# Kernel optimization log

Measured on AMD Instinct MI355X. Metric: run time of the kernel, lower is better.

## Reference

```python
import jax, jax.numpy as jnp
import numpy as np

NUM_EXPERTS = 8
TOP_K = 2
CAPACITY_FACTOR = 1.25


def setup_inputs() -> dict:
    key = jax.random.key(0)
    ks = jax.random.split(key, 5)
    B, S, D, H, E = 4, 2048, 1024, 2048, NUM_EXPERTS
    scale = 0.02
    return {
        "x": jax.random.normal(ks[0], (B, S, D), dtype=jnp.float32),
        "gate_w": jax.random.normal(ks[1], (E, D), dtype=jnp.float32) * scale,
        "gate_proj_w": jax.random.normal(ks[2], (E, H, D), dtype=jnp.float32) * scale,
        "up_proj_w": jax.random.normal(ks[3], (E, H, D), dtype=jnp.float32) * scale,
        "down_proj_w": jax.random.normal(ks[4], (E, D, H), dtype=jnp.float32) * scale,
    }


def reference(x, gate_w, gate_proj_w, up_proj_w, down_proj_w):
    B, S, D = x.shape
    E, K = NUM_EXPERTS, TOP_K
    T = B * S
    xf = x.reshape(T, D)

    # Router: softmax over expert logits, then top-k (eval mode: no aux loss)
    logits = xf @ gate_w.T                      # (T, E)
    probs = jax.nn.softmax(logits, axis=-1)
    top_p, top_i = jax.lax.top_k(probs, K)      # (T, K)
    w = top_p / (jnp.sum(top_p, axis=-1, keepdims=True) + 1e-9)  # (T, K)

    # Capacity drop: per (k, expert), keep only the first `capacity` tokens
    # in token order (matches torch loop which truncates nonzero indices).
    capacity = int(CAPACITY_FACTOR * T / E)
    oh = jax.nn.one_hot(top_i, E, dtype=jnp.int32)        # (T, K, E)
    rank = jnp.cumsum(oh, axis=0) - 1                     # rank within (k, e)
    my_rank = jnp.sum(rank * oh, axis=-1)                 # (T, K)
    keep = (my_rank < capacity).astype(w.dtype)

    # Combined per-token per-expert weight (dropped tokens get 0)
    comb = jnp.einsum("tk,tke->te", w * keep, oh.astype(w.dtype))  # (T, E)

    # Per-expert dense SwiGLU; zero-weight tokens contribute nothing,
    # which matches the masked gather/scatter-add of the original.
    out = jnp.zeros_like(xf)
    for e in range(E):
        g = jax.nn.silu(xf @ gate_proj_w[e].T)   # (T, H)
        u = xf @ up_proj_w[e].T                  # (T, H)
        y = (g * u) @ down_proj_w[e].T           # (T, D)
        out = out + comb[:, e:e + 1] * y
    return out.reshape(B, S, D)
```

## Files before the change

### kernel.cpp

```cpp
#include <hip/hip_runtime.h>
#include <hip/hip_bf16.h>
#include <stdint.h>

#define T_TOK 8192
#define D_DIM 1024
#define H_DIM 2048
#define E_NUM 8
#define CAP   1280
#define CAP2  2560

#define BM 128
#define BN 128
#define BK 32

typedef __attribute__((ext_vector_type(8))) short short8;
typedef __attribute__((ext_vector_type(4))) float float4v;
typedef __attribute__((address_space(1))) const unsigned int gu32;
typedef __attribute__((address_space(3))) unsigned int lu32;

static __device__ __forceinline__ unsigned short f2bf(float f) {
    unsigned int u = __float_as_uint(f);
    unsigned int r = (u + 0x7FFFu + ((u >> 16) & 1u)) >> 16;
    return (unsigned short)r;
}

static __device__ __forceinline__ void store4bf(unsigned short* d, float4 v) {
    union { unsigned short u[4]; uint2 q; } pk;
    pk.u[0] = f2bf(v.x); pk.u[1] = f2bf(v.y);
    pk.u[2] = f2bf(v.z); pk.u[3] = f2bf(v.w);
    *(uint2*)d = pk.q;
}

__global__ __launch_bounds__(256) void convert_all_k(
    const float* __restrict__ wg, const float* __restrict__ wu,
    const float* __restrict__ wd, const float* __restrict__ x,
    unsigned short* __restrict__ wgbf, unsigned short* __restrict__ wubf,
    unsigned short* __restrict__ wdbf, unsigned short* __restrict__ xbf) {
    const int W4 = E_NUM * H_DIM * D_DIM / 4;
    const int X4 = T_TOK * D_DIM / 4;
    const int total = 3 * W4 + X4;
    const int stride = gridDim.x * 256;
    for (int i = blockIdx.x * 256 + threadIdx.x; i < total; i += stride) {
        const float* s; unsigned short* d; int j;
        if (i < W4)            { s = wg; d = wgbf; j = i; }
        else if (i < 2 * W4)   { s = wu; d = wubf; j = i - W4; }
        else if (i < 3 * W4)   { s = wd; d = wdbf; j = i - 2 * W4; }
        else                   { s = x;  d = xbf;  j = i - 3 * W4; }
        store4bf(d + (size_t)j * 4, ((const float4*)s)[j]);
    }
}

__global__ __launch_bounds__(256) void router_k(
    const float* __restrict__ x, const float* __restrict__ gw,
    int* __restrict__ topi, float* __restrict__ topw) {
    const int t = blockIdx.x * 4 + (threadIdx.x >> 6);
    const int lane = threadIdx.x & 63;
    const float* xr = x + (size_t)t * D_DIM;

    float p[E_NUM];
#pragma unroll
    for (int e = 0; e < E_NUM; ++e) p[e] = 0.f;
#pragma unroll
    for (int c = 0; c < 4; ++c) {
        const int idx = c * 256 + lane * 4;
        const float4 xv = *(const float4*)(xr + idx);
#pragma unroll
        for (int e = 0; e < E_NUM; ++e) {
            const float4 gv = *(const float4*)(gw + e * D_DIM + idx);
            p[e] += xv.x * gv.x + xv.y * gv.y + xv.z * gv.z + xv.w * gv.w;
        }
    }
#pragma unroll
    for (int e = 0; e < E_NUM; ++e) {
        float v = p[e];
#pragma unroll
        for (int off = 32; off >= 1; off >>= 1) v += __shfl_xor(v, off);
        p[e] = v;
    }
    if (lane == 0) {
        float mx = p[0];
#pragma unroll
        for (int e = 1; e < E_NUM; ++e) mx = fmaxf(mx, p[e]);
        float pe[E_NUM]; float s = 0.f;
#pragma unroll
        for (int e = 0; e < E_NUM; ++e) { pe[e] = expf(p[e] - mx); s += pe[e]; }
        const float inv = 1.f / s;
        int i0 = 0;
#pragma unroll
        for (int e = 1; e < E_NUM; ++e) if (pe[e] > pe[i0]) i0 = e;
        int i1 = -1;
#pragma unroll
        for (int e = 0; e < E_NUM; ++e) {
            if (e == i0) continue;
            if (i1 < 0 || pe[e] > pe[i1]) i1 = e;
        }
        const float p0 = pe[i0] * inv, p1 = pe[i1] * inv;
        const float wn = 1.f / (p0 + p1 + 1e-9f);
        topi[t * 2 + 0] = i0; topi[t * 2 + 1] = i1;
        topw[t * 2 + 0] = p0 * wn; topw[t * 2 + 1] = p1 * wn;
    }
}

__global__ __launch_bounds__(1024) void assign_k(
    const int* __restrict__ topi, const float* __restrict__ topw,
    int* __restrict__ tok_list, float* __restrict__ w_list,
    int* __restrict__ n_tot) {
    __shared__ unsigned char topiL[T_TOK * 2];
    __shared__ int kept[2][E_NUM];
    __shared__ int ntotL[E_NUM];
    const int tid = threadIdx.x;
    const int wid = tid >> 6, lane = tid & 63;
    const int k = wid >> 3, e = wid & 7;
    const uint64_t lt = (1ull << lane) - 1ull;

    for (int i = tid; i < T_TOK * 2 / 4; i += 1024) {
        const int4 v = ((const int4*)topi)[i];
        uchar4 b;
        b.x = (unsigned char)v.x; b.y = (unsigned char)v.y;
        b.z = (unsigned char)v.z; b.w = (unsigned char)v.w;
        ((uchar4*)topiL)[i] = b;
    }
    __syncthreads();

    int total = 0;
    for (int base = 0; base < T_TOK; base += 64) {
        const int idx = topiL[(base + lane) * 2 + k];
        total += __popcll(__ballot(idx == e));
    }
    if (lane == 0) kept[k][e] = min(total, CAP);
    __syncthreads();
    if (tid < E_NUM) {
        ntotL[tid] = kept[0][tid] + kept[1][tid];
        n_tot[tid] = ntotL[tid];
    }
    const int myBase = e * CAP2 + (k ? kept[0][e] : 0);

    int running = 0, keptRun = 0;
    for (int base = 0; base < T_TOK; base += 64) {
        const int t = base + lane;
        const bool pred = (topiL[t * 2 + k] == e);
        const uint64_t m = __ballot(pred);
        const int rank = running + __popcll(m & lt);
        const bool keep = pred && (rank < CAP);
        const uint64_t km = __ballot(keep);
        if (keep) {
            const int slot = myBase + keptRun + __popcll(km & lt);
            tok_list[slot] = t;
            w_list[slot] = topw[t * 2 + k];
        }
        running += __popcll(m);
        keptRun += __popcll(km);
    }
    __syncthreads();
    for (int s = tid; s < E_NUM * CAP2; s += 1024) {
        const int ee = s / CAP2, ls = s - ee * CAP2;
        if (ls >= ntotL[ee]) { tok_list[s] = 0; w_list[s] = 0.f; }
    }
}

__global__ __launch_bounds__(256, 2) void gateup_bf_k(
    const unsigned short* __restrict__ xbf,
    const unsigned short* __restrict__ wgbf, const unsigned short* __restrict__ wubf,
    const int* __restrict__ tok_list, const int* __restrict__ n_tot,
    unsigned short* __restrict__ h_ws, int e0) {
    const int ez = blockIdx.z;
    const int e = e0 + ez;
    const int m0 = blockIdx.y * BM;
    if (m0 >= n_tot[e]) return;
    const int n0 = blockIdx.x * BN;

    __shared__ __align__(1024) unsigned short smem[12288];

    const int tid = threadIdx.x, wid = tid >> 6, lane = tid & 63;

    const unsigned short* gsrc[6];
    int ldsoff[6];
#pragma unroll
    for (int i = 0; i < 6; ++i) {
        const int f = (wid * 6 + i) * 64 + lane;
        const unsigned short* g;
        if (f < 512) {
            const int row = f >> 2;
            const int tok = tok_list[e * CAP2 + m0 + row];
            g = xbf + (size_t)tok * D_DIM + (f & 3) * 8;
        } else if (f < 1024) {
            const int r = (f - 512) >> 2;
            g = wgbf + ((size_t)e * H_DIM + n0 + r) * D_DIM + (f & 3) * 8;
        } else {
            const int r = (f - 1024) >> 2;
            g = wubf + ((size_t)e * H_DIM + n0 + r) * D_DIM + (f & 3) * 8;
        }
        gsrc[i] = g;
        ldsoff[i] = (wid * 6 + i) * 1024;
    }

    float4v accg[4][4], accu[4][4];
#pragma unroll
    for (int i = 0; i < 4; ++i)
#pragma unroll
        for (int j = 0; j < 4; ++j) {
            accg[i][j] = (float4v){0.f, 0.f, 0.f, 0.f};
            accu[i][j] = (float4v){0.f, 0.f, 0.f, 0.f};
        }

    const int wm = (wid & 1) * 64, wn = (wid >> 1) * 64;
    const int frow = lane & 15;
    const int fk = (lane >> 4) * 8;

    for (int k0 = 0; k0 < D_DIM; k0 += BK) {
#pragma unroll
        for (int i = 0; i < 6; ++i)
            __builtin_amdgcn_global_load_lds(
                (gu32*)(gsrc[i] + k0),
                (lu32*)((char*)smem + ldsoff[i]), 16, 0, 0);
        __syncthreads();

        short8 af[4], bgf[4], buf[4];
#pragma unroll
        for (int i = 0; i < 4; ++i)
            af[i] = *(const short8*)&smem[(wm + i * 16 + frow) * 32 + fk];
#pragma unroll
        for (int j = 0; j < 4; ++j) {
            bgf[j] = *(const short8*)&smem[4096 + (wn + j * 16 + frow) * 32 + fk];
            buf[j] = *(const short8*)&smem[8192 + (wn + j * 16 + frow) * 32 + fk];
        }
#pragma unroll
        for (int i = 0; i < 4; ++i)
#pragma unroll
            for (int j = 0; j < 4; ++j) {
                accg[i][j] = __builtin_amdgcn_mfma_f32_16x16x32_bf16(af[i], bgf[j], accg[i][j], 0, 0, 0);
                accu[i][j] = __builtin_amdgcn_mfma_f32_16x16x32_bf16(af[i], buf[j], accu[i][j], 0, 0, 0);
            }
        __syncthreads();
    }

    const int col = lane & 15, rbase = (lane >> 4) * 4;
#pragma unroll
    for (int i = 0; i < 4; ++i)
#pragma unroll
        for (int j = 0; j < 4; ++j)
#pragma unroll
            for (int r = 0; r < 4; ++r) {
                const float g = accg[i][j][r];
                const float u = accu[i][j][r];
                const float hv = (g / (1.f + __expf(-g))) * u;
                const int m = wm + i * 16 + rbase + r;
                const int n = wn + j * 16 + col;
                h_ws[((size_t)ez * CAP2 + m0 + m) * H_DIM + (n0 + n)] = f2bf(hv);
            }
}

__global__ __launch_bounds__(256, 2) void down_bf_k(
    const unsigned short* __restrict__ h_ws, const unsigned short* __restrict__ wdbf,
    const int* __restrict__ tok_list, const float* __restrict__ w_list,
    const int* __restrict__ n_tot, float* __restrict__ out, int e0) {
    const int ez = blockIdx.z;
    const int e = e0 + ez;
    const int m0 = blockIdx.y * BM;
    if (m0 >= n_tot[e]) return;
    const int n0 = blockIdx.x * BN;

    __shared__ __align__(1024) unsigned short smem[16384];
    __shared__ int tokL[BM];
    __shared__ float wL[BM];

    const int tid = threadIdx.x, wid = tid >> 6, lane = tid & 63;
    if (tid < BM) {
        tokL[tid] = tok_list[e * CAP2 + m0 + tid];
        wL[tid] = w_list[e * CAP2 + m0 + tid];
    }

    const unsigned short* gsrc[8];
    int ldsoff[8];
#pragma unroll
    for (int i = 0; i < 8; ++i) {
        const int f = (wid * 8 + i) * 64 + lane;
        const unsigned short* g;
        if (f < 1024) {
            const int r = f >> 3, c = (f & 7) ^ (r & 7);
            g = h_ws + ((size_t)ez * CAP2 + m0 + r) * H_DIM + c * 8;
        } else {
            const int fr = f - 1024;
            const int r = fr >> 3, c = (fr & 7) ^ (r & 7);
            g = wdbf + ((size_t)e * D_DIM + n0 + r) * H_DIM + c * 8;
        }
        gsrc[i] = g;
        ldsoff[i] = (wid * 8 + i) * 1024;
    }

    float4v acc[4][4];
#pragma unroll
    for (int i = 0; i < 4; ++i)
#pragma unroll
        for (int j = 0; j < 4; ++j) acc[i][j] = (float4v){0.f, 0.f, 0.f, 0.f};

    const int wm = (wid & 1) * 64, wn = (wid >> 1) * 64;
    const int frow = lane & 15;
    const int quad = lane >> 4;

    for (int k0 = 0; k0 < H_DIM; k0 += 64) {
#pragma unroll
        for (int i = 0; i < 8; ++i)
            __builtin_amdgcn_global_load_lds(
                (gu32*)(gsrc[i] + k0),
                (lu32*)((char*)smem + ldsoff[i]), 16, 0, 0);
        __syncthreads();

        short8 af[2][4], bf[2][4];
#pragma unroll
        for (int s = 0; s < 2; ++s) {
            const int c = s * 4 + quad;
#pragma unroll
            for (int i = 0; i < 4; ++i) {
                const int row = wm + i * 16 + frow;
                af[s][i] = *(const short8*)&smem[(row * 8 + (c ^ (row & 7))) * 8];
            }
#pragma unroll
            for (int j = 0; j < 4; ++j) {
                const int row = wn + j * 16 + frow;
                bf[s][j] = *(const short8*)&smem[8192 + (row * 8 + (c ^ (row & 7))) * 8];
            }
        }
#pragma unroll
        for (int s = 0; s < 2; ++s)
#pragma unroll
            for (int i = 0; i < 4; ++i)
#pragma unroll
                for (int j = 0; j < 4; ++j)
                    acc[i][j] = __builtin_amdgcn_mfma_f32_16x16x32_bf16(af[s][i], bf[s][j], acc[i][j], 0, 0, 0);
        __syncthreads();
    }

    const int col = lane & 15, rbase = (lane >> 4) * 4;
#pragma unroll
    for (int i = 0; i < 4; ++i)
#pragma unroll
        for (int j = 0; j < 4; ++j)
#pragma unroll
            for (int r = 0; r < 4; ++r) {
                const int m = wm + i * 16 + rbase + r;
                const int n = wn + j * 16 + col;
                const float v = acc[i][j][r] * wL[m];
                unsafeAtomicAdd(&out[(size_t)tokL[m] * D_DIM + n0 + n], v);
            }
}

__global__ __launch_bounds__(256, 2) void gateup_legacy_k(
    const float* __restrict__ x,
    const float* __restrict__ wg_all, const float* __restrict__ wu_all,
    const int* __restrict__ tok_list, const int* __restrict__ n_tot,
    unsigned short* __restrict__ h_ws, int e0) {
    const int ez = blockIdx.z;
    const int e = e0 + ez;
    const int m0 = blockIdx.y * BM;
    if (m0 >= n_tot[e]) return;
    const int n0 = blockIdx.x * BN;

    __shared__ __align__(16) unsigned short As[BM][BK];
    __shared__ __align__(16) unsigned short Bg[BN][BK];
    __shared__ __align__(16) unsigned short Bu[BN][BK];
    __shared__ int tokL[BM];

    const int tid = threadIdx.x;
    if (tid < BM) tokL[tid] = tok_list[e * CAP2 + m0 + tid];
    __syncthreads();

    const float* wg = wg_all + (size_t)e * H_DIM * D_DIM;
    const float* wu = wu_all + (size_t)e * H_DIM * D_DIM;

    const float* aSrc[4]; const float* gSrc[4]; const float* uSrc[4];
    unsigned short* aDst[4]; unsigned short* gDst[4]; unsigned short* uDst[4];
#pragma unroll
    for (int it = 0; it < 4; ++it) {
        const int fid = it * 256 + tid;
        const int row = fid >> 3;
        const int c4 = (fid & 7) * 4;
        aSrc[it] = x + (size_t)tokL[row] * D_DIM + c4;
        gSrc[it] = wg + (size_t)(n0 + row) * D_DIM + c4;
        uSrc[it] = wu + (size_t)(n0 + row) * D_DIM + c4;
        aDst[it] = &As[row][c4];
        gDst[it] = &Bg[row][c4];
        uDst[it] = &Bu[row][c4];
    }

    float4v accg[4][4], accu[4][4];
#pragma unroll
    for (int i = 0; i < 4; ++i)
#pragma unroll
        for (int j = 0; j < 4; ++j) {
            accg[i][j] = (float4v){0.f, 0.f, 0.f, 0.f};
            accu[i][j] = (float4v){0.f, 0.f, 0.f, 0.f};
        }

    const int wid = tid >> 6, lane = tid & 63;
    const int wm = (wid & 1) * 64, wn = (wid >> 1) * 64;
    const int frow = lane & 15;
    const int fk = (lane >> 4) * 8;

    for (int k0 = 0; k0 < D_DIM; k0 += BK) {
#pragma unroll
        for (int it = 0; it < 4; ++it) {
            store4bf(aDst[it], *(const float4*)(aSrc[it] + k0));
            store4bf(gDst[it], *(const float4*)(gSrc[it] + k0));
            store4bf(uDst[it], *(const float4*)(uSrc[it] + k0));
        }
        __syncthreads();
        short8 af[4], bgf[4], buf[4];
#pragma unroll
        for (int i = 0; i < 4; ++i)
            af[i] = *(const short8*)&As[wm + i * 16 + frow][fk];
#pragma unroll
        for (int j = 0; j < 4; ++j) {
            bgf[j] = *(const short8*)&Bg[wn + j * 16 + frow][fk];
            buf[j] = *(const short8*)&Bu[wn + j * 16 + frow][fk];
        }
#pragma unroll
        for (int i = 0; i < 4; ++i)
#pragma unroll
            for (int j = 0; j < 4; ++j) {
                accg[i][j] = __builtin_amdgcn_mfma_f32_16x16x32_bf16(af[i], bgf[j], accg[i][j], 0, 0, 0);
                accu[i][j] = __builtin_amdgcn_mfma_f32_16x16x32_bf16(af[i], buf[j], accu[i][j], 0, 0, 0);
            }
        __syncthreads();
    }

    const int col = lane & 15, rbase = (lane >> 4) * 4;
#pragma unroll
    for (int i = 0; i < 4; ++i)
#pragma unroll
        for (int j = 0; j < 4; ++j)
#pragma unroll
            for (int r = 0; r < 4; ++r) {
                const float g = accg[i][j][r];
                const float u = accu[i][j][r];
                const float hv = (g / (1.f + __expf(-g))) * u;
                const int m = wm + i * 16 + rbase + r;
                const int n = wn + j * 16 + col;
                h_ws[((size_t)ez * CAP2 + m0 + m) * H_DIM + (n0 + n)] = f2bf(hv);
            }
}

__global__ __launch_bounds__(256, 2) void down_legacy_k(
    const unsigned short* __restrict__ h_ws, const float* __restrict__ wd_all,
    const int* __restrict__ tok_list, const float* __restrict__ w_list,
    const int* __restrict__ n_tot, float* __restrict__ out, int e0) {
    const int ez = blockIdx.z;
    const int e = e0 + ez;
    const int m0 = blockIdx.y * BM;
    if (m0 >= n_tot[e]) return;
    const int n0 = blockIdx.x * BN;

    __shared__ __align__(16) unsigned short As[BM][BK];
    __shared__ __align__(16) unsigned short Bs[BN][BK];
    __shared__ int tokL[BM];
    __shared__ float wL[BM];

    const int tid = threadIdx.x;
    if (tid < BM) {
        tokL[tid] = tok_list[e * CAP2 + m0 + tid];
        wL[tid] = w_list[e * CAP2 + m0 + tid];
    }
    __syncthreads();

    const unsigned short* hA = h_ws + ((size_t)ez * CAP2 + m0) * H_DIM;
    const float* wd = wd_all + (size_t)e * D_DIM * H_DIM;

    const unsigned short* aSrc[2]; unsigned short* aDst[2];
#pragma unroll
    for (int it = 0; it < 2; ++it) {
        const int fid = it * 256 + tid;
        const int row = fid >> 2;
        const int c8 = (fid & 3) * 8;
        aSrc[it] = hA + (size_t)row * H_DIM + c8;
        aDst[it] = &As[row][c8];
    }
    const float* bSrc[4]; unsigned short* bDst[4];
#pragma unroll
    for (int it = 0; it < 4; ++it) {
        const int fid = it * 256 + tid;
        const int row = fid >> 3;
        const int c4 = (fid & 7) * 4;
        bSrc[it] = wd + (size_t)(n0 + row) * H_DIM + c4;
        bDst[it] = &Bs[row][c4];
    }

    float4v acc[4][4];
#pragma unroll
    for (int i = 0; i < 4; ++i)
#pragma unroll
        for (int j = 0; j < 4; ++j) acc[i][j] = (float4v){0.f, 0.f, 0.f, 0.f};

    const int wid = tid >> 6, lane = tid & 63;
    const int wm = (wid & 1) * 64, wn = (wid >> 1) * 64;
    const int frow = lane & 15;
    const int fk = (lane >> 4) * 8;

    for (int k0 = 0; k0 < H_DIM; k0 += BK) {
#pragma unroll
        for (int it = 0; it < 2; ++it)
            *(uint4*)aDst[it] = *(const uint4*)(aSrc[it] + k0);
#pragma unroll
        for (int it = 0; it < 4; ++it)
            store4bf(bDst[it], *(const float4*)(bSrc[it] + k0));
        __syncthreads();
        short8 af[4], bf[4];
#pragma unroll
        for (int i = 0; i < 4; ++i)
            af[i] = *(const short8*)&As[wm + i * 16 + frow][fk];
#pragma unroll
        for (int j = 0; j < 4; ++j)
            bf[j] = *(const short8*)&Bs[wn + j * 16 + frow][fk];
#pragma unroll
        for (int i = 0; i < 4; ++i)
#pragma unroll
            for (int j = 0; j < 4; ++j)
                acc[i][j] = __builtin_amdgcn_mfma_f32_16x16x32_bf16(af[i], bf[j], acc[i][j], 0, 0, 0);
        __syncthreads();
    }

    const int col = lane & 15, rbase = (lane >> 4) * 4;
#pragma unroll
    for (int i = 0; i < 4; ++i)
#pragma unroll
        for (int j = 0; j < 4; ++j)
#pragma unroll
            for (int r = 0; r < 4; ++r) {
                const int m = wm + i * 16 + rbase + r;
                const int n = wn + j * 16 + col;
                const float v = acc[i][j][r] * wL[m];
                unsafeAtomicAdd(&out[(size_t)tokL[m] * D_DIM + n0 + n], v);
            }
}

extern "C" void kernel_launch(void* const* d_in, const int* in_sizes, int n_in,
                              void* d_out, int out_size, void* d_ws, size_t ws_size,
                              hipStream_t stream) {
    const float* x        = (const float*)d_in[0];
    const float* gate_w   = (const float*)d_in[1];
    const float* gate_pw  = (const float*)d_in[2];
    const float* up_pw    = (const float*)d_in[3];
    const float* down_pw  = (const float*)d_in[4];
    float* out = (float*)d_out;
    (void)n_in; (void)in_sizes; (void)out_size;

    uint8_t* ws = (uint8_t*)d_ws;
    size_t off = 0;
    int*   topi     = (int*)(ws + off);   off += (size_t)T_TOK * 2 * 4;
    float* topw     = (float*)(ws + off); off += (size_t)T_TOK * 2 * 4;
    int*   tok_list = (int*)(ws + off);   off += (size_t)E_NUM * CAP2 * 4;
    float* w_list   = (float*)(ws + off); off += (size_t)E_NUM * CAP2 * 4;
    int*   n_tot    = (int*)(ws + off);   off += 256;
    off = (off + 4095) & ~(size_t)4095;
    const size_t routing_end = off;

    const size_t x_elems = (size_t)T_TOK * D_DIM;
    const size_t w_elems = (size_t)E_NUM * H_DIM * D_DIM;
    unsigned short* xbf  = (unsigned short*)(ws + off); off += x_elems * 2;
    unsigned short* wgbf = (unsigned short*)(ws + off); off += w_elems * 2;
    unsigned short* wubf = (unsigned short*)(ws + off); off += w_elems * 2;
    unsigned short* wdbf = (unsigned short*)(ws + off); off += w_elems * 2;
    const size_t need_base = off;
    const size_t per_e = (size_t)CAP2 * H_DIM * 2;

    hipMemsetAsync(out, 0, (size_t)T_TOK * D_DIM * sizeof(float), stream);
    router_k<<<T_TOK / 4, 256, 0, stream>>>(x, gate_w, topi, topw);
    assign_k<<<1, 1024, 0, stream>>>(topi, topw, tok_list, w_list, n_tot);

    if (ws_size >= need_base + per_e) {
        unsigned short* h_ws = (unsigned short*)(ws + need_base);
        int chunk = (int)((ws_size - need_base) / per_e);
        if (chunk > E_NUM) chunk = E_NUM;

        convert_all_k<<<4096, 256, 0, stream>>>(gate_pw, up_pw, down_pw, x,
                                                wgbf, wubf, wdbf, xbf);

        for (int e0 = 0; e0 < E_NUM; e0 += chunk) {
            const int ne = (e0 + chunk <= E_NUM) ? chunk : (E_NUM - e0);
            dim3 g1(H_DIM / BN, CAP2 / BM, ne);
            gateup_bf_k<<<g1, 256, 0, stream>>>(xbf, wgbf, wubf, tok_list, n_tot, h_ws, e0);
            dim3 g2(D_DIM / BN, CAP2 / BM, ne);
            down_bf_k<<<g2, 256, 0, stream>>>(h_ws, wdbf, tok_list, w_list, n_tot, out, e0);
        }
    } else {
        unsigned short* h_ws = (unsigned short*)(ws + routing_end);
        int chunk = (ws_size > routing_end) ? (int)((ws_size - routing_end) / per_e) : 0;
        if (chunk > E_NUM) chunk = E_NUM;
        if (chunk < 1) chunk = 1;

        for (int e0 = 0; e0 < E_NUM; e0 += chunk) {
            const int ne = (e0 + chunk <= E_NUM) ? chunk : (E_NUM - e0);
            dim3 g1(H_DIM / BN, CAP2 / BM, ne);
            gateup_legacy_k<<<g1, 256, 0, stream>>>(x, gate_pw, up_pw, tok_list, n_tot, h_ws, e0);
            dim3 g2(D_DIM / BN, CAP2 / BM, ne);
            down_legacy_k<<<g2, 256, 0, stream>>>(h_ws, down_pw, tok_list, w_list, n_tot, out, e0);
        }
    }
}
```

Measured before the change: 671.8 us.

## Split expert slots per top-k and replace down-projection atomics with stores

Token slots for each expert are now split into fixed halves per top-k choice. The down-projection runs in two launches: the k=0 launch writes outputs with plain stores, and the k=1 launch does a non-atomic read-add. This is valid because each token maps to at most one expert per k, and it removes the global atomic adds. The bf16 conversion of x also moves into the router kernel, so x is read once instead of twice. In exchange there is an extra launch and padding per k-half, and the down kernel now has a per-row bounds check.

```diff
diff --git a/kernel.cpp b/kernel.cpp
--- a/kernel.cpp
+++ b/kernel.cpp
@@ -8,6 +8,7 @@
 #define E_NUM 8
 #define CAP   1280
 #define CAP2  2560
+#define MT_K  10
 
 #define BM 128
 #define BN 128
@@ -31,31 +32,31 @@
     *(uint2*)d = pk.q;
 }
 
-__global__ __launch_bounds__(256) void convert_all_k(
+__global__ __launch_bounds__(256) void convert_w_k(
     const float* __restrict__ wg, const float* __restrict__ wu,
-    const float* __restrict__ wd, const float* __restrict__ x,
+    const float* __restrict__ wd,
     unsigned short* __restrict__ wgbf, unsigned short* __restrict__ wubf,
-    unsigned short* __restrict__ wdbf, unsigned short* __restrict__ xbf) {
+    unsigned short* __restrict__ wdbf) {
     const int W4 = E_NUM * H_DIM * D_DIM / 4;
-    const int X4 = T_TOK * D_DIM / 4;
-    const int total = 3 * W4 + X4;
+    const int total = 3 * W4;
     const int stride = gridDim.x * 256;
     for (int i = blockIdx.x * 256 + threadIdx.x; i < total; i += stride) {
         const float* s; unsigned short* d; int j;
-        if (i < W4)            { s = wg; d = wgbf; j = i; }
-        else if (i < 2 * W4)   { s = wu; d = wubf; j = i - W4; }
-        else if (i < 3 * W4)   { s = wd; d = wdbf; j = i - 2 * W4; }
-        else                   { s = x;  d = xbf;  j = i - 3 * W4; }
+        if (i < W4)          { s = wg; d = wgbf; j = i; }
+        else if (i < 2 * W4) { s = wu; d = wubf; j = i - W4; }
+        else                 { s = wd; d = wdbf; j = i - 2 * W4; }
         store4bf(d + (size_t)j * 4, ((const float4*)s)[j]);
     }
 }
 
 __global__ __launch_bounds__(256) void router_k(
     const float* __restrict__ x, const float* __restrict__ gw,
-    int* __restrict__ topi, float* __restrict__ topw) {
+    int* __restrict__ topi, float* __restrict__ topw,
+    unsigned short* __restrict__ xbf) {
     const int t = blockIdx.x * 4 + (threadIdx.x >> 6);
     const int lane = threadIdx.x & 63;
     const float* xr = x + (size_t)t * D_DIM;
+    unsigned short* xbr = xbf + (size_t)t * D_DIM;
 
     float p[E_NUM];
 #pragma unroll
@@ -64,6 +65,7 @@
     for (int c = 0; c < 4; ++c) {
         const int idx = c * 256 + lane * 4;
         const float4 xv = *(const float4*)(xr + idx);
+        store4bf(xbr + idx, xv);
 #pragma unroll
         for (int e = 0; e < E_NUM; ++e) {
             const float4 gv = *(const float4*)(gw + e * D_DIM + idx);
@@ -104,10 +106,9 @@
 __global__ __launch_bounds__(1024) void assign_k(
     const int* __restrict__ topi, const float* __restrict__ topw,
     int* __restrict__ tok_list, float* __restrict__ w_list,
-    int* __restrict__ n_tot) {
+    int* __restrict__ cnt) {
     __shared__ unsigned char topiL[T_TOK * 2];
     __shared__ int kept[2][E_NUM];
-    __shared__ int ntotL[E_NUM];
     const int tid = threadIdx.x;
     const int wid = tid >> 6, lane = tid & 63;
     const int k = wid >> 3, e = wid & 7;
@@ -127,13 +128,13 @@
         const int idx = topiL[(base + lane) * 2 + k];
         total += __popcll(__ballot(idx == e));
     }
-    if (lane == 0) kept[k][e] = min(total, CAP);
+    if (lane == 0) {
+        const int kc = min(total, CAP);
+        kept[k][e] = kc;
+        cnt[e * 2 + k] = kc;
+    }
     __syncthreads();
-    if (tid < E_NUM) {
-        ntotL[tid] = kept[0][tid] + kept[1][tid];
-        n_tot[tid] = ntotL[tid];
-    }
-    const int myBase = e * CAP2 + (k ? kept[0][e] : 0);
+    const int myBase = e * CAP2 + k * CAP;
 
     int running = 0, keptRun = 0;
     for (int base = 0; base < T_TOK; base += 64) {
@@ -153,21 +154,26 @@
     }
     __syncthreads();
     for (int s = tid; s < E_NUM * CAP2; s += 1024) {
-        const int ee = s / CAP2, ls = s - ee * CAP2;
-        if (ls >= ntotL[ee]) { tok_list[s] = 0; w_list[s] = 0.f; }
+        const int ee = s / CAP2;
+        const int rem = s - ee * CAP2;
+        const int kk = rem / CAP, ls = rem - kk * CAP;
+        if (ls >= kept[kk][ee]) { tok_list[s] = 0; w_list[s] = 0.f; }
     }
 }
 
 __global__ __launch_bounds__(256, 2) void gateup_bf_k(
     const unsigned short* __restrict__ xbf,
     const unsigned short* __restrict__ wgbf, const unsigned short* __restrict__ wubf,
-    const int* __restrict__ tok_list, const int* __restrict__ n_tot,
+    const int* __restrict__ tok_list, const int* __restrict__ cnt,
     unsigned short* __restrict__ h_ws, int e0) {
     const int ez = blockIdx.z;
     const int e = e0 + ez;
-    const int m0 = blockIdx.y * BM;
-    if (m0 >= n_tot[e]) return;
+    const int kk = blockIdx.y / MT_K;
+    const int m0 = (blockIdx.y - kk * MT_K) * BM;
+    if (m0 >= cnt[e * 2 + kk]) return;
     const int n0 = blockIdx.x * BN;
+    const int sbase = e * CAP2 + kk * CAP + m0;
+    const size_t hbase = (size_t)ez * CAP2 + kk * CAP + m0;
 
     __shared__ __align__(1024) unsigned short smem[12288];
 
@@ -181,7 +187,7 @@
         const unsigned short* g;
         if (f < 512) {
             const int row = f >> 2;
-            const int tok = tok_list[e * CAP2 + m0 + row];
+            const int tok = tok_list[sbase + row];
             g = xbf + (size_t)tok * D_DIM + (f & 3) * 8;
         } else if (f < 1024) {
             const int r = (f - 512) >> 2;
@@ -246,19 +252,22 @@
                 const float hv = (g / (1.f + __expf(-g))) * u;
                 const int m = wm + i * 16 + rbase + r;
                 const int n = wn + j * 16 + col;
-                h_ws[((size_t)ez * CAP2 + m0 + m) * H_DIM + (n0 + n)] = f2bf(hv);
+                h_ws[(hbase + m) * H_DIM + (n0 + n)] = f2bf(hv);
             }
 }
 
 __global__ __launch_bounds__(256, 2) void down_bf_k(
     const unsigned short* __restrict__ h_ws, const unsigned short* __restrict__ wdbf,
     const int* __restrict__ tok_list, const float* __restrict__ w_list,
-    const int* __restrict__ n_tot, float* __restrict__ out, int e0) {
+    const int* __restrict__ cnt, float* __restrict__ out, int e0, int kk) {
     const int ez = blockIdx.z;
     const int e = e0 + ez;
     const int m0 = blockIdx.y * BM;
-    if (m0 >= n_tot[e]) return;
+    const int nkept = cnt[e * 2 + kk];
+    if (m0 >= nkept) return;
     const int n0 = blockIdx.x * BN;
+    const int sbase = e * CAP2 + kk * CAP + m0;
+    const size_t hbase = (size_t)ez * CAP2 + kk * CAP + m0;
 
     __shared__ __align__(1024) unsigned short smem[16384];
     __shared__ int tokL[BM];
@@ -266,8 +275,8 @@
 
     const int tid = threadIdx.x, wid = tid >> 6, lane = tid & 63;
     if (tid < BM) {
-        tokL[tid] = tok_list[e * CAP2 + m0 + tid];
-        wL[tid] = w_list[e * CAP2 + m0 + tid];
+        tokL[tid] = tok_list[sbase + tid];
+        wL[tid] = w_list[sbase + tid];
     }
 
     const unsigned short* gsrc[8];
@@ -278,7 +287,7 @@
         const unsigned short* g;
         if (f < 1024) {
             const int r = f >> 3, c = (f & 7) ^ (r & 7);
-            g = h_ws + ((size_t)ez * CAP2 + m0 + r) * H_DIM + c * 8;
+            g = h_ws + (hbase + r) * H_DIM + c * 8;
         } else {
             const int fr = f - 1024;
             const int r = fr >> 3, c = (fr & 7) ^ (r & 7);
@@ -335,26 +344,34 @@
 #pragma unroll
     for (int i = 0; i < 4; ++i)
 #pragma unroll
-        for (int j = 0; j < 4; ++j)
-#pragma unroll
-            for (int r = 0; r < 4; ++r) {
-                const int m = wm + i * 16 + rbase + r;
-                const int n = wn + j * 16 + col;
-                const float v = acc[i][j][r] * wL[m];
-                unsafeAtomicAdd(&out[(size_t)tokL[m] * D_DIM + n0 + n], v);
-            }
+        for (int r = 0; r < 4; ++r) {
+            const int m = wm + i * 16 + rbase + r;
+            if (m0 + m >= nkept) continue;
+            const float wRow = wL[m];
+            float* orow = out + (size_t)tokL[m] * D_DIM + n0;
+#pragma unroll
+            for (int j = 0; j < 4; ++j) {
+                const int n = j * 16 + wn + col;
+                const float v = acc[i][j][r] * wRow;
+                if (kk == 0) orow[n] = v;
+                else         orow[n] += v;
+            }
+        }
 }
 
 __global__ __launch_bounds__(256, 2) void gateup_legacy_k(
     const float* __restrict__ x,
     const float* __restrict__ wg_all, const float* __restrict__ wu_all,
-    const int* __restrict__ tok_list, const int* __restrict__ n_tot,
+    const int* __restrict__ tok_list, const int* __restrict__ cnt,
     unsigned short* __restrict__ h_ws, int e0) {
     const int ez = blockIdx.z;
     const int e = e0 + ez;
-    const int m0 = blockIdx.y * BM;
-    if (m0 >= n_tot[e]) return;
+    const int kk = blockIdx.y / MT_K;
+    const int m0 = (blockIdx.y - kk * MT_K) * BM;
+    if (m0 >= cnt[e * 2 + kk]) return;
     const int n0 = blockIdx.x * BN;
+    const int sbase = e * CAP2 + kk * CAP + m0;
+    const size_t hbase = (size_t)ez * CAP2 + kk * CAP + m0;
 
     __shared__ __align__(16) unsigned short As[BM][BK];
     __shared__ __align__(16) unsigned short Bg[BN][BK];
@@ -362,7 +379,7 @@
     __shared__ int tokL[BM];
 
     const int tid = threadIdx.x;
-    if (tid < BM) tokL[tid] = tok_list[e * CAP2 + m0 + tid];
+    if (tid < BM) tokL[tid] = tok_list[sbase + tid];
     __syncthreads();
 
     const float* wg = wg_all + (size_t)e * H_DIM * D_DIM;
@@ -436,19 +453,22 @@
                 const float hv = (g / (1.f + __expf(-g))) * u;
                 const int m = wm + i * 16 + rbase + r;
                 const int n = wn + j * 16 + col;
-                h_ws[((size_t)ez * CAP2 + m0 + m) * H_DIM + (n0 + n)] = f2bf(hv);
+                h_ws[(hbase + m) * H_DIM + (n0 + n)] = f2bf(hv);
             }
 }
 
 __global__ __launch_bounds__(256, 2) void down_legacy_k(
     const unsigned short* __restrict__ h_ws, const float* __restrict__ wd_all,
     const int* __restrict__ tok_list, const float* __restrict__ w_list,
-    const int* __restrict__ n_tot, float* __restrict__ out, int e0) {
+    const int* __restrict__ cnt, float* __restrict__ out, int e0) {
     const int ez = blockIdx.z;
     const int e = e0 + ez;
-    const int m0 = blockIdx.y * BM;
-    if (m0 >= n_tot[e]) return;
+    const int kk = blockIdx.y / MT_K;
+    const int m0 = (blockIdx.y - kk * MT_K) * BM;
+    if (m0 >= cnt[e * 2 + kk]) return;
     const int n0 = blockIdx.x * BN;
+    const int sbase = e * CAP2 + kk * CAP + m0;
+    const size_t hbase = (size_t)ez * CAP2 + kk * CAP + m0;
 
     __shared__ __align__(16) unsigned short As[BM][BK];
     __shared__ __align__(16) unsigned short Bs[BN][BK];
@@ -457,12 +477,12 @@
 
     const int tid = threadIdx.x;
     if (tid < BM) {
-        tokL[tid] = tok_list[e * CAP2 + m0 + tid];
-        wL[tid] = w_list[e * CAP2 + m0 + tid];
+        tokL[tid] = tok_list[sbase + tid];
+        wL[tid] = w_list[sbase + tid];
     }
     __syncthreads();
 
-    const unsigned short* hA = h_ws + ((size_t)ez * CAP2 + m0) * H_DIM;
+    const unsigned short* hA = h_ws + hbase * H_DIM;
     const float* wd = wd_all + (size_t)e * D_DIM * H_DIM;
 
     const unsigned short* aSrc[2]; unsigned short* aDst[2];
@@ -549,7 +569,7 @@
     float* topw     = (float*)(ws + off); off += (size_t)T_TOK * 2 * 4;
     int*   tok_list = (int*)(ws + off);   off += (size_t)E_NUM * CAP2 * 4;
     float* w_list   = (float*)(ws + off); off += (size_t)E_NUM * CAP2 * 4;
-    int*   n_tot    = (int*)(ws + off);   off += 256;
+    int*   cnt      = (int*)(ws + off);   off += 256;
     off = (off + 4095) & ~(size_t)4095;
     const size_t routing_end = off;
 
@@ -563,23 +583,24 @@
     const size_t per_e = (size_t)CAP2 * H_DIM * 2;
 
     hipMemsetAsync(out, 0, (size_t)T_TOK * D_DIM * sizeof(float), stream);
-    router_k<<<T_TOK / 4, 256, 0, stream>>>(x, gate_w, topi, topw);
-    assign_k<<<1, 1024, 0, stream>>>(topi, topw, tok_list, w_list, n_tot);
 
     if (ws_size >= need_base + per_e) {
         unsigned short* h_ws = (unsigned short*)(ws + need_base);
         int chunk = (int)((ws_size - need_base) / per_e);
         if (chunk > E_NUM) chunk = E_NUM;
 
-        convert_all_k<<<4096, 256, 0, stream>>>(gate_pw, up_pw, down_pw, x,
-                                                wgbf, wubf, wdbf, xbf);
+        router_k<<<T_TOK / 4, 256, 0, stream>>>(x, gate_w, topi, topw, xbf);
+        assign_k<<<1, 1024, 0, stream>>>(topi, topw, tok_list, w_list, cnt);
+        convert_w_k<<<4096, 256, 0, stream>>>(gate_pw, up_pw, down_pw,
+                                              wgbf, wubf, wdbf);
 
         for (int e0 = 0; e0 < E_NUM; e0 += chunk) {
             const int ne = (e0 + chunk <= E_NUM) ? chunk : (E_NUM - e0);
-            dim3 g1(H_DIM / BN, CAP2 / BM, ne);
-            gateup_bf_k<<<g1, 256, 0, stream>>>(xbf, wgbf, wubf, tok_list, n_tot, h_ws, e0);
-            dim3 g2(D_DIM / BN, CAP2 / BM, ne);
-            down_bf_k<<<g2, 256, 0, stream>>>(h_ws, wdbf, tok_list, w_list, n_tot, out, e0);
+            dim3 g1(H_DIM / BN, 2 * MT_K, ne);
+            gateup_bf_k<<<g1, 256, 0, stream>>>(xbf, wgbf, wubf, tok_list, cnt, h_ws, e0);
+            dim3 g2(D_DIM / BN, MT_K, ne);
+            down_bf_k<<<g2, 256, 0, stream>>>(h_ws, wdbf, tok_list, w_list, cnt, out, e0, 0);
+            down_bf_k<<<g2, 256, 0, stream>>>(h_ws, wdbf, tok_list, w_list, cnt, out, e0, 1);
         }
     } else {
         unsigned short* h_ws = (unsigned short*)(ws + routing_end);
@@ -587,12 +608,15 @@
         if (chunk > E_NUM) chunk = E_NUM;
         if (chunk < 1) chunk = 1;
 
+        router_k<<<T_TOK / 4, 256, 0, stream>>>(x, gate_w, topi, topw, xbf);
+        assign_k<<<1, 1024, 0, stream>>>(topi, topw, tok_list, w_list, cnt);
+
         for (int e0 = 0; e0 < E_NUM; e0 += chunk) {
             const int ne = (e0 + chunk <= E_NUM) ? chunk : (E_NUM - e0);
-            dim3 g1(H_DIM / BN, CAP2 / BM, ne);
-            gateup_legacy_k<<<g1, 256, 0, stream>>>(x, gate_pw, up_pw, tok_list, n_tot, h_ws, e0);
-            dim3 g2(D_DIM / BN, CAP2 / BM, ne);
-            down_legacy_k<<<g2, 256, 0, stream>>>(h_ws, down_pw, tok_list, w_list, n_tot, out, e0);
-        }
-    }
-}
+            dim3 g1(H_DIM / BN, 2 * MT_K, ne);
+            gateup_legacy_k<<<g1, 256, 0, stream>>>(x, gate_pw, up_pw, tok_list, cnt, h_ws, e0);
+            dim3 g2(D_DIM / BN, 2 * MT_K, ne);
+            down_legacy_k<<<g2, 256, 0, stream>>>(h_ws, down_pw, tok_list, w_list, cnt, out, e0);
+        }
+    }
+}
```

After: 639.8 us. 4.8% less time.
